# Kernel tuning notes

Hardware: AMD Instinct MI355X
Metric: run time of the kernel (lower is better)

## Reference

```python
import jax, jax.numpy as jnp
import numpy as np

LOG2PI = 1.8378770664093453
KL_WEIGHT = 1.0
N_OBS = 2_000_000
N_REFL = 250_000
N_IMG = 2000
MC = 32
N_OPS = 2
D_META = 6
D_EMB = 32
D_IN = 2 + 2 + D_META + 2 + D_EMB  # Imodel(2) + Iscale(2) + metadata(6) + wavelength + 1/d^2 + image embed
HIDDEN = 64


def weighted_pearson(x, y, w):
    z = 1.0 / w.sum(-1)
    mx = z * (w * x).sum(-1)
    my = z * (w * y).sum(-1)
    dx = x - mx
    dy = y - my
    cxy = z * (w * dx * dy).sum(-1)
    cx = z * (w * dx * dx).sum(-1)
    cy = z * (w * dy * dy).sum(-1)
    return cxy / jnp.sqrt(cx * cy)


def setup_inputs() -> dict:
    key = jax.random.key(0)
    ks = jax.random.split(key, 16)
    I = jax.random.normal(ks[0], (N_OBS, 1), jnp.float32)
    SigI = jax.random.uniform(ks[1], (N_OBS, 1), jnp.float32, 0.5, 1.5)
    image_id = jnp.sort(jax.random.randint(ks[2], (N_OBS,), 0, N_IMG, jnp.int32))
    metadata = jax.random.normal(ks[3], (N_OBS, D_META), jnp.float32)
    wavelength = 1.0 + 0.1 * jax.random.uniform(ks[4], (N_OBS, 1), jnp.float32)
    dHKL = jax.random.uniform(ks[5], (N_OBS, 1), jnp.float32, 1.0, 4.0)
    refl_ids = jax.random.randint(ks[6], (N_OPS, N_OBS), 0, N_REFL, jnp.int32)
    q_loc = jax.random.normal(ks[7], (N_REFL,), jnp.float32)
    q_scale_raw = 0.1 * jax.random.normal(ks[8], (N_REFL,), jnp.float32)
    img_emb = 0.1 * jax.random.normal(ks[9], (N_IMG, D_EMB), jnp.float32)
    W1 = jax.random.normal(ks[10], (D_IN, HIDDEN), jnp.float32) / np.sqrt(D_IN)
    b1 = jnp.zeros((HIDDEN,), jnp.float32)
    W2 = jax.random.normal(ks[11], (HIDDEN, 2), jnp.float32) / np.sqrt(HIDDEN)
    b2 = jnp.zeros((2,), jnp.float32)
    zeps = jax.random.normal(ks[12], (MC, N_REFL), jnp.float32)
    seps = jax.random.normal(ks[13], (N_OBS, MC), jnp.float32)
    return dict(I=I, SigI=SigI, image_id=image_id, metadata=metadata,
                wavelength=wavelength, dHKL=dHKL, refl_ids=refl_ids,
                q_loc=q_loc, q_scale_raw=q_scale_raw, img_emb=img_emb,
                W1=W1, b1=b1, W2=W2, b2=b2, zeps=zeps, seps=seps)


def reference(I, SigI, image_id, metadata, wavelength, dHKL, refl_ids,
              q_loc, q_scale_raw, img_emb, W1, b1, W2, b2, zeps, seps):
    n_images = img_emb.shape[0]
    sq = jax.nn.softplus(q_scale_raw)                         # q.stddev  [n_refl]
    # KL(N(q_loc, sq) || N(0, 1)), analytic, averaged over reflections
    kl_div = (-jnp.log(sq) + 0.5 * (sq * sq + q_loc * q_loc) - 0.5).mean()
    meta = jnp.concatenate([metadata, wavelength, 1.0 / jnp.square(dHKL)], -1)  # [N, 8]
    Iscale = jnp.concatenate([I, SigI], -1)                   # [N, 2]
    Imodel = jnp.stack([q_loc, sq], -1)                       # [n_refl, 2]
    zT = (q_loc[None, :] + sq[None, :] * zeps).T              # rsample, [n_refl, mc]
    emb = img_emb[image_id]                                   # [N, d_emb]
    ll_list, Ipred_list = [], []
    for op in range(refl_ids.shape[0]):                       # small fixed op count
        rid = refl_ids[op]                                    # [N]
        _Imodel = Imodel[rid]                                 # gather  [N, 2]
        feats = jnp.concatenate([_Imodel, Iscale, meta, emb], -1)
        h = jax.nn.relu(feats @ W1 + b1)
        loc_ls = h @ W2 + b2                                  # [N, 2]
        scale = loc_ls[:, :1] + jax.nn.softplus(loc_ls[:, 1:]) * seps  # [N, mc]
        _Ipred = zT[rid] * scale                              # gather * scale [N, mc]
        _ll = -0.5 * jnp.square((_Ipred - I) / SigI) - jnp.log(SigI) - 0.5 * LOG2PI
        _ll = jax.ops.segment_sum(_ll, image_id, num_segments=n_images)  # [n_img, mc]
        ll_list.append(_ll.mean(-1))                          # [n_img]
        Ipred_list.append(_Ipred.mean(-1))                    # [N]
    ll = jnp.stack(ll_list, -1)                               # [n_img, n_ops]
    ll_max = ll.max(-1)
    op_idx = ll.argmax(-1)                                    # [n_img]
    elbo = -ll_max.mean() + KL_WEIGHT * kl_div
    Ipred = jnp.stack(Ipred_list, -1)                         # [N, n_ops]
    sel = jnp.take_along_axis(Ipred, op_idx[image_id][:, None], -1)[:, 0]
    w = 1.0 / jnp.square(SigI)
    cc = weighted_pearson(I[:, 0], sel, w[:, 0])
    return jnp.stack([elbo, cc])
```

## Files before the change

kernel.cpp:

```cpp
#include <hip/hip_runtime.h>
#include <math.h>

#define N_OBS_C 2000000
#define N_REFL_C 250000
#define N_IMG_C 2000
#define MC_C 32
#define HID 64
#define NSLOT 16
#define LOG2PI_F 1.8378770664093453f


typedef float f2 __attribute__((ext_vector_type(2)));

__device__ __forceinline__ void pkfma(f2& d, f2 a, f2 b) {
    asm("v_pk_fma_f32 %0, %1, %2, %0" : "+v"(d) : "v"(a), "v"(b));
}
__device__ __forceinline__ f2 pkfma3(f2 a, f2 b, f2 c) {
    f2 d;
    asm("v_pk_fma_f32 %0, %1, %2, %3" : "=v"(d) : "v"(a), "v"(b), "v"(c));
    return d;
}

__device__ __forceinline__ float softplusf(float x) {
    return (x > 20.f) ? x : log1pf(expf(x));
}

#define ZERO_F4 96004
__global__ __launch_bounds__(256) void k_zero(float4* __restrict__ p) {
    int i = blockIdx.x * 256 + threadIdx.x;
    if (i < ZERO_F4) p[i] = make_float4(0.f, 0.f, 0.f, 0.f);
}

__global__ __launch_bounds__(256) void k_refl(const float* __restrict__ q_loc,
                                              const float* __restrict__ q_scale_raw,
                                              const float* __restrict__ zeps,
                                              float* __restrict__ sq,
                                              float* __restrict__ zT,
                                              double* __restrict__ kl_sum) {
    int r = blockIdx.x * 256 + threadIdx.x;
    double kl = 0.0;
    if (r < N_REFL_C) {
        float ql = q_loc[r];
        float sp = softplusf(q_scale_raw[r]);
        sq[r] = sp;
        kl = (double)(-logf(sp) + 0.5f * (sp * sp + ql * ql) - 0.5f);
        float z[MC_C];
#pragma unroll
        for (int m = 0; m < MC_C; ++m)
            z[m] = fmaf(sp, zeps[(size_t)m * N_REFL_C + r], ql);
        float4* outp = (float4*)(zT + (size_t)r * MC_C);
#pragma unroll
        for (int q = 0; q < MC_C / 4; ++q)
            outp[q] = make_float4(z[4 * q], z[4 * q + 1], z[4 * q + 2], z[4 * q + 3]);
    }
    for (int o = 32; o > 0; o >>= 1) kl += __shfl_xor(kl, o);
    __shared__ double skl[4];
    int lane = threadIdx.x & 63, w = threadIdx.x >> 6;
    if (lane == 0) skl[w] = kl;
    __syncthreads();
    if (threadIdx.x == 0) atomicAdd(kl_sum, skl[0] + skl[1] + skl[2] + skl[3]);
}

__global__ __launch_bounds__(64) void k_imgpre(const float* __restrict__ img_emb,
                                               const float* __restrict__ W1,
                                               const float* __restrict__ b1,
                                               float* __restrict__ img_pre) {
    int g = blockIdx.x;
    int j = threadIdx.x;
    float acc = b1[j];
#pragma unroll
    for (int e = 0; e < 32; ++e)
        acc = fmaf(img_emb[g * 32 + e], W1[(12 + e) * HID + j], acc);
    img_pre[g * HID + j] = acc;
}

__global__ __launch_bounds__(256) void k_mlp(const float* __restrict__ I,
                                             const float* __restrict__ SigI,
                                             const int* __restrict__ image_id,
                                             const float* __restrict__ metadata,
                                             const float* __restrict__ wavelength,
                                             const float* __restrict__ dHKL,
                                             const int* __restrict__ refl_ids,
                                             const float* __restrict__ q_loc,
                                             const float* __restrict__ W1,
                                             const float* __restrict__ W2,
                                             const float* __restrict__ b2,
                                             const float* __restrict__ sq,
                                             const float* __restrict__ img_pre,
                                             float4* __restrict__ params) {
    __shared__ float sW1[12 * HID];
    __shared__ float sW2a[HID], sW2b[HID];
    for (int t = threadIdx.x; t < 12 * HID; t += 256) sW1[t] = W1[t];
    if (threadIdx.x < HID) {
        sW2a[threadIdx.x] = W2[threadIdx.x * 2 + 0];
        sW2b[threadIdx.x] = W2[threadIdx.x * 2 + 1];
    }
    __syncthreads();

    int n0 = blockIdx.x * 512 + threadIdx.x;
    int n1 = n0 + 256;
    bool a0 = (n0 < N_OBS_C), a1 = (n1 < N_OBS_C);
    int m0 = a0 ? n0 : (N_OBS_C - 1);
    int m1 = a1 ? n1 : (N_OBS_C - 1);

    f2 f0p[10], f1p[10];
    {
        float v;
        v = I[m0];            f0p[0].x = v; f0p[0].y = v;
        v = SigI[m0];         f0p[1].x = v; f0p[1].y = v;
#pragma unroll
        for (int i = 0; i < 6; ++i) {
            v = metadata[(size_t)m0 * 6 + i];
            f0p[2 + i].x = v; f0p[2 + i].y = v;
        }
        v = wavelength[m0];   f0p[8].x = v; f0p[8].y = v;
        float dh = dHKL[m0];
        v = 1.0f / (dh * dh); f0p[9].x = v; f0p[9].y = v;

        v = I[m1];            f1p[0].x = v; f1p[0].y = v;
        v = SigI[m1];         f1p[1].x = v; f1p[1].y = v;
#pragma unroll
        for (int i = 0; i < 6; ++i) {
            v = metadata[(size_t)m1 * 6 + i];
            f1p[2 + i].x = v; f1p[2 + i].y = v;
        }
        v = wavelength[m1];   f1p[8].x = v; f1p[8].y = v;
        dh = dHKL[m1];
        v = 1.0f / (dh * dh); f1p[9].x = v; f1p[9].y = v;
    }

    int g0 = image_id[m0], g1 = image_id[m1];
    int r00 = refl_ids[m0], r01 = refl_ids[N_OBS_C + m0];
    int r10 = refl_ids[m1], r11 = refl_ids[N_OBS_C + m1];
    f2 qa0p, sa0p, qb0p, sb0p, qa1p, sa1p, qb1p, sb1p;
    { float v;
      v = q_loc[r00]; qa0p.x = v; qa0p.y = v;
      v = sq[r00];    sa0p.x = v; sa0p.y = v;
      v = q_loc[r01]; qb0p.x = v; qb0p.y = v;
      v = sq[r01];    sb0p.x = v; sb0p.y = v;
      v = q_loc[r10]; qa1p.x = v; qa1p.y = v;
      v = sq[r10];    sa1p.x = v; sa1p.y = v;
      v = q_loc[r11]; qb1p.x = v; qb1p.y = v;
      v = sq[r11];    sb1p.x = v; sb1p.y = v;
    }
    const float* ip0 = img_pre + (size_t)g0 * HID;
    const float* ip1 = img_pre + (size_t)g1 * HID;

    f2 lA00 = {0.f, 0.f}, lA01 = {0.f, 0.f}, lB00 = {0.f, 0.f}, lB01 = {0.f, 0.f};
    f2 lA10 = {0.f, 0.f}, lA11 = {0.f, 0.f}, lB10 = {0.f, 0.f}, lB11 = {0.f, 0.f};

#pragma unroll 1
    for (int jt = 0; jt < HID; jt += 8) {
        f2 ac0[4], ac1[4];
        {
            float4 pa = *(const float4*)&ip0[jt];
            float4 pb = *(const float4*)&ip0[jt + 4];
            ac0[0].x = pa.x; ac0[0].y = pa.y;
            ac0[1].x = pa.z; ac0[1].y = pa.w;
            ac0[2].x = pb.x; ac0[2].y = pb.y;
            ac0[3].x = pb.z; ac0[3].y = pb.w;
            pa = *(const float4*)&ip1[jt];
            pb = *(const float4*)&ip1[jt + 4];
            ac1[0].x = pa.x; ac1[0].y = pa.y;
            ac1[1].x = pa.z; ac1[1].y = pa.w;
            ac1[2].x = pb.x; ac1[2].y = pb.y;
            ac1[3].x = pb.z; ac1[3].y = pb.w;
        }
#pragma unroll
        for (int i = 0; i < 10; ++i) {
            float4 wa = *(const float4*)&sW1[(i + 2) * HID + jt];
            float4 wb = *(const float4*)&sW1[(i + 2) * HID + jt + 4];
            f2 w0; w0.x = wa.x; w0.y = wa.y;
            f2 w1; w1.x = wa.z; w1.y = wa.w;
            f2 w2; w2.x = wb.x; w2.y = wb.y;
            f2 w3; w3.x = wb.z; w3.y = wb.w;
            pkfma(ac0[0], f0p[i], w0); pkfma(ac1[0], f1p[i], w0);
            pkfma(ac0[1], f0p[i], w1); pkfma(ac1[1], f1p[i], w1);
            pkfma(ac0[2], f0p[i], w2); pkfma(ac1[2], f1p[i], w2);
            pkfma(ac0[3], f0p[i], w3); pkfma(ac1[3], f1p[i], w3);
        }
        f2 w0p[4], w1p[4], vap[4], vbp[4];
        {
            float4 wa = *(const float4*)&sW1[jt];
            float4 wb = *(const float4*)&sW1[jt + 4];
            w0p[0].x = wa.x; w0p[0].y = wa.y;
            w0p[1].x = wa.z; w0p[1].y = wa.w;
            w0p[2].x = wb.x; w0p[2].y = wb.y;
            w0p[3].x = wb.z; w0p[3].y = wb.w;
            wa = *(const float4*)&sW1[HID + jt];
            wb = *(const float4*)&sW1[HID + jt + 4];
            w1p[0].x = wa.x; w1p[0].y = wa.y;
            w1p[1].x = wa.z; w1p[1].y = wa.w;
            w1p[2].x = wb.x; w1p[2].y = wb.y;
            w1p[3].x = wb.z; w1p[3].y = wb.w;
            wa = *(const float4*)&sW2a[jt];
            wb = *(const float4*)&sW2a[jt + 4];
            vap[0].x = wa.x; vap[0].y = wa.y;
            vap[1].x = wa.z; vap[1].y = wa.w;
            vap[2].x = wb.x; vap[2].y = wb.y;
            vap[3].x = wb.z; vap[3].y = wb.w;
            wa = *(const float4*)&sW2b[jt];
            wb = *(const float4*)&sW2b[jt + 4];
            vbp[0].x = wa.x; vbp[0].y = wa.y;
            vbp[1].x = wa.z; vbp[1].y = wa.w;
            vbp[2].x = wb.x; vbp[2].y = wb.y;
            vbp[3].x = wb.z; vbp[3].y = wb.w;
        }
#pragma unroll
        for (int k = 0; k < 4; ++k) {
            f2 h;
            h = pkfma3(sa0p, w1p[k], ac0[k]);
            pkfma(h, qa0p, w0p[k]);
            h.x = fmaxf(h.x, 0.f); h.y = fmaxf(h.y, 0.f);
            pkfma(lA00, h, vap[k]);
            pkfma(lA01, h, vbp[k]);
            h = pkfma3(sb0p, w1p[k], ac0[k]);
            pkfma(h, qb0p, w0p[k]);
            h.x = fmaxf(h.x, 0.f); h.y = fmaxf(h.y, 0.f);
            pkfma(lB00, h, vap[k]);
            pkfma(lB01, h, vbp[k]);
            h = pkfma3(sa1p, w1p[k], ac1[k]);
            pkfma(h, qa1p, w0p[k]);
            h.x = fmaxf(h.x, 0.f); h.y = fmaxf(h.y, 0.f);
            pkfma(lA10, h, vap[k]);
            pkfma(lA11, h, vbp[k]);
            h = pkfma3(sb1p, w1p[k], ac1[k]);
            pkfma(h, qb1p, w0p[k]);
            h.x = fmaxf(h.x, 0.f); h.y = fmaxf(h.y, 0.f);
            pkfma(lB10, h, vap[k]);
            pkfma(lB11, h, vbp[k]);
        }
    }

    float bb0 = b2[0], bb1 = b2[1];
    if (a0) {
        float la0 = bb0 + lA00.x + lA00.y;
        float la1 = bb1 + lA01.x + lA01.y;
        float lb0 = bb0 + lB00.x + lB00.y;
        float lb1 = bb1 + lB01.x + lB01.y;
        params[n0] = make_float4(la0, softplusf(la1), lb0, softplusf(lb1));
    }
    if (a1) {
        float la0 = bb0 + lA10.x + lA10.y;
        float la1 = bb1 + lA11.x + lA11.y;
        float lb0 = bb0 + lB10.x + lB10.y;
        float lb1 = bb1 + lB11.x + lB11.y;
        params[n1] = make_float4(la0, softplusf(la1), lb0, softplusf(lb1));
    }
}

__global__ __launch_bounds__(256) void k_mc(const float* __restrict__ I,
                                            const float* __restrict__ SigI,
                                            const int* __restrict__ image_id,
                                            const int* __restrict__ refl_ids,
                                            const float4* __restrict__ params,
                                            const float* __restrict__ seps,
                                            const float* __restrict__ zT,
                                            float* __restrict__ img_mom) {
    int t = threadIdx.x;
    int grp = t >> 3;
    int m4 = t & 7;
    int n = blockIdx.x * 32 + grp;

    float In = I[n];
    float Sn = SigI[n];
    int g = image_id[n];
    int rid0 = refl_ids[n];
    int rid1 = refl_ids[N_OBS_C + n];
    float4 pp = params[n];

    float4 ss = *(const float4*)&seps[(size_t)n * MC_C + m4 * 4];
    float4 z0 = *(const float4*)&zT[(size_t)rid0 * MC_C + m4 * 4];
    float4 z1 = *(const float4*)&zT[(size_t)rid1 * MC_C + m4 * 4];

    float rsig = 1.0f / Sn;
    float mnIr = -In * rsig;

    float sd20 = 0.f, sip0 = 0.f, sd21 = 0.f, sip1 = 0.f;
#define MCSTEP(zc0, zc1, sc_)                              \
    {                                                      \
        float sc0 = fmaf(pp.y, sc_, pp.x);                 \
        float ip0 = zc0 * sc0;                             \
        float d0 = fmaf(ip0, rsig, mnIr);                  \
        sd20 = fmaf(d0, d0, sd20);                         \
        sip0 += ip0;                                       \
        float sc1 = fmaf(pp.w, sc_, pp.z);                 \
        float ip1 = zc1 * sc1;                             \
        float d1 = fmaf(ip1, rsig, mnIr);                  \
        sd21 = fmaf(d1, d1, sd21);                         \
        sip1 += ip1;                                       \
    }
    MCSTEP(z0.x, z1.x, ss.x)
    MCSTEP(z0.y, z1.y, ss.y)
    MCSTEP(z0.z, z1.z, ss.z)
    MCSTEP(z0.w, z1.w, ss.w)
#undef MCSTEP

#pragma unroll
    for (int o = 4; o > 0; o >>= 1) {
        sd20 += __shfl_xor(sd20, o);
        sd21 += __shfl_xor(sd21, o);
        sip0 += __shfl_xor(sip0, o);
        sip1 += __shfl_xor(sip1, o);
    }

    __shared__ float mom[12][33];
    __shared__ int sg[32];
    if (m4 == 0) {
        float logS32 = 32.f * logf(Sn) + 16.f * LOG2PI_F;
        float y0 = sip0 * (1.0f / 32.0f);
        float y1 = sip1 * (1.0f / 32.0f);
        float w = rsig * rsig;
        mom[0][grp] = -0.5f * sd20 - logS32;
        mom[1][grp] = -0.5f * sd21 - logS32;
        mom[2][grp] = w;
        mom[3][grp] = w * In;
        mom[4][grp] = w * In * In;
        mom[5][grp] = w * y0;
        mom[6][grp] = w * y0 * y0;
        mom[7][grp] = w * In * y0;
        mom[8][grp] = w * y1;
        mom[9][grp] = w * y1 * y1;
        mom[10][grp] = w * In * y1;
        mom[11][grp] = 0.f;
        sg[grp] = g;
    }
    __syncthreads();
    if (t < 64) {
        int s = t & 31;
        int half = t >> 5;
        int gs = sg[s];
        int gfirst = sg[0];
        unsigned long long bal = __ballot(gs == gfirst);
        bool allsame = (bal == 0xFFFFFFFFFFFFFFFFull);
        int slot = blockIdx.x & (NSLOT - 1);
#pragma unroll
        for (int jj = 0; jj < 6; ++jj) {
            int j = jj * 2 + half;
            float v = mom[j][s];
            if (allsame) {
#pragma unroll
                for (int o = 16; o > 0; o >>= 1) v += __shfl_xor(v, o);
                if (s == 0) atomicAdd(&img_mom[(gfirst * 12 + j) * NSLOT + slot], v);
            } else {
                atomicAdd(&img_mom[(gs * 12 + j) * NSLOT + slot], v);
            }
        }
    }
}

__global__ __launch_bounds__(256) void k_img(const float* __restrict__ img_mom,
                                             double* __restrict__ accs) {
    int g = blockIdx.x * 256 + threadIdx.x;
    double red7[7] = {0, 0, 0, 0, 0, 0, 0};
    if (g < N_IMG_C) {
        float M[12];
#pragma unroll
        for (int j = 0; j < 12; ++j) {
            const float4* p = (const float4*)&img_mom[(g * 12 + j) * NSLOT];
            float4 q0 = p[0], q1 = p[1], q2 = p[2], q3 = p[3];
            M[j] = (q0.x + q0.y + q0.z + q0.w) + (q1.x + q1.y + q1.z + q1.w) +
                   (q2.x + q2.y + q2.z + q2.w) + (q3.x + q3.y + q3.z + q3.w);
        }
        float ll0 = M[0] * (1.0f / 32.0f);
        float ll1 = M[1] * (1.0f / 32.0f);
        bool op1 = (ll1 > ll0);
        red7[0] = (double)fmaxf(ll0, ll1);
        red7[1] = (double)M[2];
        red7[2] = (double)M[3];
        red7[3] = (double)(op1 ? M[8] : M[5]);
        red7[4] = (double)M[4];
        red7[5] = (double)(op1 ? M[9] : M[6]);
        red7[6] = (double)(op1 ? M[10] : M[7]);
    }
#pragma unroll
    for (int k = 0; k < 7; ++k)
        for (int o = 32; o > 0; o >>= 1) red7[k] += __shfl_xor(red7[k], o);
    __shared__ double sred[4][7];
    int lane = threadIdx.x & 63, w = threadIdx.x >> 6;
    if (lane == 0) {
#pragma unroll
        for (int k = 0; k < 7; ++k) sred[w][k] = red7[k];
    }
    __syncthreads();
    if (threadIdx.x < 7) {
        double v = sred[0][threadIdx.x] + sred[1][threadIdx.x] +
                   sred[2][threadIdx.x] + sred[3][threadIdx.x];
        atomicAdd(&accs[1 + threadIdx.x], v);
    }
}

__global__ void k_final(const double* __restrict__ accs, float* __restrict__ out) {
    double kl = accs[0] / (double)N_REFL_C;
    double elbo = -(accs[1] / (double)N_IMG_C) + 1.0 * kl;
    double W = accs[2], Sx = accs[3], Sy = accs[4];
    double Sxx = accs[5], Syy = accs[6], Sxy = accs[7];
    double z = 1.0 / W;
    double mx = z * Sx, my = z * Sy;
    double cxy = z * Sxy - mx * my;
    double cx = z * Sxx - mx * mx;
    double cy = z * Syy - my * my;
    double cc = cxy / sqrt(cx * cy);
    out[0] = (float)elbo;
    out[1] = (float)cc;
}

extern "C" void kernel_launch(void* const* d_in, const int* in_sizes, int n_in,
                              void* d_out, int out_size, void* d_ws, size_t ws_size,
                              hipStream_t stream) {
    const float* I = (const float*)d_in[0];
    const float* SigI = (const float*)d_in[1];
    const int* image_id = (const int*)d_in[2];
    const float* metadata = (const float*)d_in[3];
    const float* wavelength = (const float*)d_in[4];
    const float* dHKL = (const float*)d_in[5];
    const int* refl_ids = (const int*)d_in[6];
    const float* q_loc = (const float*)d_in[7];
    const float* q_scale_raw = (const float*)d_in[8];
    const float* img_emb = (const float*)d_in[9];
    const float* W1 = (const float*)d_in[10];
    const float* b1 = (const float*)d_in[11];
    const float* W2 = (const float*)d_in[12];
    const float* b2 = (const float*)d_in[13];
    const float* zeps = (const float*)d_in[14];
    const float* seps = (const float*)d_in[15];
    float* out = (float*)d_out;

    char* ws = (char*)d_ws;
    double* accs = (double*)ws;
    float* img_mom = (float*)(ws + 64);
    float* sqv = (float*)(ws + 2097152);
    float* img_pre = (float*)(ws + 4194304);
    float* zT = (float*)(ws + 8388608);
    float4* params = (float4*)(ws + 50331648);

    k_zero<<<(ZERO_F4 + 255) / 256, 256, 0, stream>>>((float4*)ws);
    k_refl<<<(N_REFL_C + 255) / 256, 256, 0, stream>>>(q_loc, q_scale_raw, zeps,
                                                       sqv, zT, &accs[0]);
    k_imgpre<<<N_IMG_C, 64, 0, stream>>>(img_emb, W1, b1, img_pre);
    k_mlp<<<(N_OBS_C + 511) / 512, 256, 0, stream>>>(I, SigI, image_id, metadata,
                                                     wavelength, dHKL, refl_ids,
                                                     q_loc, W1, W2, b2, sqv,
                                                     img_pre, params);
    k_mc<<<N_OBS_C / 32, 256, 0, stream>>>(I, SigI, image_id, refl_ids,
                                           params, seps, zT, img_mom);
    k_img<<<(N_IMG_C + 255) / 256, 256, 0, stream>>>(img_mom, accs);
    k_final<<<1, 1, 0, stream>>>(accs, out);
}
```

Baseline: 287.8 us.

## Fuse MLP and Monte Carlo kernels via shared-memory params and block-local image reduction

Merges the per-observation MLP kernel and the Monte Carlo likelihood kernel into one kernel. The per-observation params now stay in shared memory, so the params array is no longer written to and re-read from global memory. Each thread now handles one observation instead of two. Image moment partial sums are accumulated with shared-memory atomics, indexed relative to the block's first image, and flushed once per block; images at offset 32 or more fall back to global atomics. The costs are halved ILP in the MLP section, more shared-memory atomics, and extra sync and occupancy pressure in the fused kernel.

```diff
diff --git a/kernel.cpp b/kernel.cpp
--- a/kernel.cpp
+++ b/kernel.cpp
@@ -74,97 +74,82 @@
     img_pre[g * HID + j] = acc;
 }
 
-__global__ __launch_bounds__(256) void k_mlp(const float* __restrict__ I,
-                                             const float* __restrict__ SigI,
-                                             const int* __restrict__ image_id,
-                                             const float* __restrict__ metadata,
-                                             const float* __restrict__ wavelength,
-                                             const float* __restrict__ dHKL,
-                                             const int* __restrict__ refl_ids,
-                                             const float* __restrict__ q_loc,
-                                             const float* __restrict__ W1,
-                                             const float* __restrict__ W2,
-                                             const float* __restrict__ b2,
-                                             const float* __restrict__ sq,
-                                             const float* __restrict__ img_pre,
-                                             float4* __restrict__ params) {
+__global__ __launch_bounds__(256) void k_main(const float* __restrict__ I,
+                                              const float* __restrict__ SigI,
+                                              const int* __restrict__ image_id,
+                                              const float* __restrict__ metadata,
+                                              const float* __restrict__ wavelength,
+                                              const float* __restrict__ dHKL,
+                                              const int* __restrict__ refl_ids,
+                                              const float* __restrict__ q_loc,
+                                              const float* __restrict__ W1,
+                                              const float* __restrict__ W2,
+                                              const float* __restrict__ b2,
+                                              const float* __restrict__ sq,
+                                              const float* __restrict__ img_pre,
+                                              const float* __restrict__ seps,
+                                              const float* __restrict__ zT,
+                                              float* __restrict__ img_mom) {
     __shared__ float sW1[12 * HID];
     __shared__ float sW2a[HID], sW2b[HID];
-    for (int t = threadIdx.x; t < 12 * HID; t += 256) sW1[t] = W1[t];
-    if (threadIdx.x < HID) {
-        sW2a[threadIdx.x] = W2[threadIdx.x * 2 + 0];
-        sW2b[threadIdx.x] = W2[threadIdx.x * 2 + 1];
-    }
-    __syncthreads();
-
-    int n0 = blockIdx.x * 512 + threadIdx.x;
-    int n1 = n0 + 256;
-    bool a0 = (n0 < N_OBS_C), a1 = (n1 < N_OBS_C);
-    int m0 = a0 ? n0 : (N_OBS_C - 1);
-    int m1 = a1 ? n1 : (N_OBS_C - 1);
-
-    f2 f0p[10], f1p[10];
+    __shared__ float4 pms[256];
+    __shared__ float2 sIS[256];
+    __shared__ int2 srid[256];
+    __shared__ int sgid[256];
+    __shared__ float lmom[32][12];
+
+    int tid = threadIdx.x;
+    for (int t = tid; t < 12 * HID; t += 256) sW1[t] = W1[t];
+    if (tid < HID) {
+        sW2a[tid] = W2[tid * 2 + 0];
+        sW2b[tid] = W2[tid * 2 + 1];
+    }
+    for (int t = tid; t < 32 * 12; t += 256) ((float*)lmom)[t] = 0.f;
+
+    int n = blockIdx.x * 256 + tid;
+    bool act = (n < N_OBS_C);
+    int m = act ? n : (N_OBS_C - 1);
+
+    float Inv = I[m];
+    float Snv = SigI[m];
+    f2 fp[10];
     {
         float v;
-        v = I[m0];            f0p[0].x = v; f0p[0].y = v;
-        v = SigI[m0];         f0p[1].x = v; f0p[1].y = v;
+        fp[0].x = Inv; fp[0].y = Inv;
+        fp[1].x = Snv; fp[1].y = Snv;
 #pragma unroll
         for (int i = 0; i < 6; ++i) {
-            v = metadata[(size_t)m0 * 6 + i];
-            f0p[2 + i].x = v; f0p[2 + i].y = v;
-        }
-        v = wavelength[m0];   f0p[8].x = v; f0p[8].y = v;
-        float dh = dHKL[m0];
-        v = 1.0f / (dh * dh); f0p[9].x = v; f0p[9].y = v;
-
-        v = I[m1];            f1p[0].x = v; f1p[0].y = v;
-        v = SigI[m1];         f1p[1].x = v; f1p[1].y = v;
-#pragma unroll
-        for (int i = 0; i < 6; ++i) {
-            v = metadata[(size_t)m1 * 6 + i];
-            f1p[2 + i].x = v; f1p[2 + i].y = v;
-        }
-        v = wavelength[m1];   f1p[8].x = v; f1p[8].y = v;
-        dh = dHKL[m1];
-        v = 1.0f / (dh * dh); f1p[9].x = v; f1p[9].y = v;
-    }
-
-    int g0 = image_id[m0], g1 = image_id[m1];
-    int r00 = refl_ids[m0], r01 = refl_ids[N_OBS_C + m0];
-    int r10 = refl_ids[m1], r11 = refl_ids[N_OBS_C + m1];
-    f2 qa0p, sa0p, qb0p, sb0p, qa1p, sa1p, qb1p, sb1p;
+            v = metadata[(size_t)m * 6 + i];
+            fp[2 + i].x = v; fp[2 + i].y = v;
+        }
+        v = wavelength[m]; fp[8].x = v; fp[8].y = v;
+        float dh = dHKL[m];
+        v = 1.0f / (dh * dh); fp[9].x = v; fp[9].y = v;
+    }
+    int g = image_id[m];
+    int r0 = refl_ids[m];
+    int r1 = refl_ids[N_OBS_C + m];
+    f2 qa, sa, qb, sb;
     { float v;
-      v = q_loc[r00]; qa0p.x = v; qa0p.y = v;
-      v = sq[r00];    sa0p.x = v; sa0p.y = v;
-      v = q_loc[r01]; qb0p.x = v; qb0p.y = v;
-      v = sq[r01];    sb0p.x = v; sb0p.y = v;
-      v = q_loc[r10]; qa1p.x = v; qa1p.y = v;
-      v = sq[r10];    sa1p.x = v; sa1p.y = v;
-      v = q_loc[r11]; qb1p.x = v; qb1p.y = v;
-      v = sq[r11];    sb1p.x = v; sb1p.y = v;
-    }
-    const float* ip0 = img_pre + (size_t)g0 * HID;
-    const float* ip1 = img_pre + (size_t)g1 * HID;
-
-    f2 lA00 = {0.f, 0.f}, lA01 = {0.f, 0.f}, lB00 = {0.f, 0.f}, lB01 = {0.f, 0.f};
-    f2 lA10 = {0.f, 0.f}, lA11 = {0.f, 0.f}, lB10 = {0.f, 0.f}, lB11 = {0.f, 0.f};
+      v = q_loc[r0]; qa.x = v; qa.y = v;
+      v = sq[r0];    sa.x = v; sa.y = v;
+      v = q_loc[r1]; qb.x = v; qb.y = v;
+      v = sq[r1];    sb.x = v; sb.y = v;
+    }
+    const float* ipg = img_pre + (size_t)g * HID;
+
+    f2 lA0 = {0.f, 0.f}, lA1 = {0.f, 0.f}, lB0 = {0.f, 0.f}, lB1 = {0.f, 0.f};
 
 #pragma unroll 1
     for (int jt = 0; jt < HID; jt += 8) {
-        f2 ac0[4], ac1[4];
+        f2 ac[4];
         {
-            float4 pa = *(const float4*)&ip0[jt];
-            float4 pb = *(const float4*)&ip0[jt + 4];
-            ac0[0].x = pa.x; ac0[0].y = pa.y;
-            ac0[1].x = pa.z; ac0[1].y = pa.w;
-            ac0[2].x = pb.x; ac0[2].y = pb.y;
-            ac0[3].x = pb.z; ac0[3].y = pb.w;
-            pa = *(const float4*)&ip1[jt];
-            pb = *(const float4*)&ip1[jt + 4];
-            ac1[0].x = pa.x; ac1[0].y = pa.y;
-            ac1[1].x = pa.z; ac1[1].y = pa.w;
-            ac1[2].x = pb.x; ac1[2].y = pb.y;
-            ac1[3].x = pb.z; ac1[3].y = pb.w;
+            float4 pa = *(const float4*)&ipg[jt];
+            float4 pb = *(const float4*)&ipg[jt + 4];
+            ac[0].x = pa.x; ac[0].y = pa.y;
+            ac[1].x = pa.z; ac[1].y = pa.w;
+            ac[2].x = pb.x; ac[2].y = pb.y;
+            ac[3].x = pb.z; ac[3].y = pb.w;
         }
 #pragma unroll
         for (int i = 0; i < 10; ++i) {
@@ -174,10 +159,10 @@
             f2 w1; w1.x = wa.z; w1.y = wa.w;
             f2 w2; w2.x = wb.x; w2.y = wb.y;
             f2 w3; w3.x = wb.z; w3.y = wb.w;
-            pkfma(ac0[0], f0p[i], w0); pkfma(ac1[0], f1p[i], w0);
-            pkfma(ac0[1], f0p[i], w1); pkfma(ac1[1], f1p[i], w1);
-            pkfma(ac0[2], f0p[i], w2); pkfma(ac1[2], f1p[i], w2);
-            pkfma(ac0[3], f0p[i], w3); pkfma(ac1[3], f1p[i], w3);
+            pkfma(ac[0], fp[i], w0);
+            pkfma(ac[1], fp[i], w1);
+            pkfma(ac[2], fp[i], w2);
+            pkfma(ac[3], fp[i], w3);
         }
         f2 w0p[4], w1p[4], vap[4], vbp[4];
         {
@@ -209,142 +194,114 @@
 #pragma unroll
         for (int k = 0; k < 4; ++k) {
             f2 h;
-            h = pkfma3(sa0p, w1p[k], ac0[k]);
-            pkfma(h, qa0p, w0p[k]);
+            h = pkfma3(sa, w1p[k], ac[k]);
+            pkfma(h, qa, w0p[k]);
             h.x = fmaxf(h.x, 0.f); h.y = fmaxf(h.y, 0.f);
-            pkfma(lA00, h, vap[k]);
-            pkfma(lA01, h, vbp[k]);
-            h = pkfma3(sb0p, w1p[k], ac0[k]);
-            pkfma(h, qb0p, w0p[k]);
+            pkfma(lA0, h, vap[k]);
+            pkfma(lA1, h, vbp[k]);
+            h = pkfma3(sb, w1p[k], ac[k]);
+            pkfma(h, qb, w0p[k]);
             h.x = fmaxf(h.x, 0.f); h.y = fmaxf(h.y, 0.f);
-            pkfma(lB00, h, vap[k]);
-            pkfma(lB01, h, vbp[k]);
-            h = pkfma3(sa1p, w1p[k], ac1[k]);
-            pkfma(h, qa1p, w0p[k]);
-            h.x = fmaxf(h.x, 0.f); h.y = fmaxf(h.y, 0.f);
-            pkfma(lA10, h, vap[k]);
-            pkfma(lA11, h, vbp[k]);
-            h = pkfma3(sb1p, w1p[k], ac1[k]);
-            pkfma(h, qb1p, w0p[k]);
-            h.x = fmaxf(h.x, 0.f); h.y = fmaxf(h.y, 0.f);
-            pkfma(lB10, h, vap[k]);
-            pkfma(lB11, h, vbp[k]);
-        }
-    }
-
-    float bb0 = b2[0], bb1 = b2[1];
-    if (a0) {
-        float la0 = bb0 + lA00.x + lA00.y;
-        float la1 = bb1 + lA01.x + lA01.y;
-        float lb0 = bb0 + lB00.x + lB00.y;
-        float lb1 = bb1 + lB01.x + lB01.y;
-        params[n0] = make_float4(la0, softplusf(la1), lb0, softplusf(lb1));
-    }
-    if (a1) {
-        float la0 = bb0 + lA10.x + lA10.y;
-        float la1 = bb1 + lA11.x + lA11.y;
-        float lb0 = bb0 + lB10.x + lB10.y;
-        float lb1 = bb1 + lB11.x + lB11.y;
-        params[n1] = make_float4(la0, softplusf(la1), lb0, softplusf(lb1));
-    }
-}
-
-__global__ __launch_bounds__(256) void k_mc(const float* __restrict__ I,
-                                            const float* __restrict__ SigI,
-                                            const int* __restrict__ image_id,
-                                            const int* __restrict__ refl_ids,
-                                            const float4* __restrict__ params,
-                                            const float* __restrict__ seps,
-                                            const float* __restrict__ zT,
-                                            float* __restrict__ img_mom) {
-    int t = threadIdx.x;
-    int grp = t >> 3;
-    int m4 = t & 7;
-    int n = blockIdx.x * 32 + grp;
-
-    float In = I[n];
-    float Sn = SigI[n];
-    int g = image_id[n];
-    int rid0 = refl_ids[n];
-    int rid1 = refl_ids[N_OBS_C + n];
-    float4 pp = params[n];
-
-    float4 ss = *(const float4*)&seps[(size_t)n * MC_C + m4 * 4];
-    float4 z0 = *(const float4*)&zT[(size_t)rid0 * MC_C + m4 * 4];
-    float4 z1 = *(const float4*)&zT[(size_t)rid1 * MC_C + m4 * 4];
-
-    float rsig = 1.0f / Sn;
-    float mnIr = -In * rsig;
-
-    float sd20 = 0.f, sip0 = 0.f, sd21 = 0.f, sip1 = 0.f;
+            pkfma(lB0, h, vap[k]);
+            pkfma(lB1, h, vbp[k]);
+        }
+    }
+
+    {
+        float bb0 = b2[0], bb1 = b2[1];
+        float la0 = bb0 + lA0.x + lA0.y;
+        float la1 = bb1 + lA1.x + lA1.y;
+        float lb0 = bb0 + lB0.x + lB0.y;
+        float lb1 = bb1 + lB1.x + lB1.y;
+        pms[tid] = make_float4(la0, softplusf(la1), lb0, softplusf(lb1));
+        sIS[tid] = make_float2(Inv, Snv);
+        srid[tid] = make_int2(r0, r1);
+        sgid[tid] = act ? g : -1;
+    }
+    __syncthreads();
+
+    int grp = tid >> 3;
+    int m4 = tid & 7;
+    int gmin = sgid[0];
+    int slot = blockIdx.x & (NSLOT - 1);
+
+#pragma unroll 2
+    for (int c = 0; c < 8; ++c) {
+        int o = c * 32 + grp;
+        int gb = sgid[o];
+        int2 rr = srid[o];
+        float4 pp = pms[o];
+        float2 IS = sIS[o];
+        int nb = (gb >= 0) ? (blockIdx.x * 256 + o) : 0;
+
+        float4 ss = *(const float4*)&seps[(size_t)nb * MC_C + m4 * 4];
+        float4 z0 = *(const float4*)&zT[(size_t)rr.x * MC_C + m4 * 4];
+        float4 z1 = *(const float4*)&zT[(size_t)rr.y * MC_C + m4 * 4];
+
+        float rsig = 1.0f / IS.y;
+        float mnIr = -IS.x * rsig;
+
+        float sd20 = 0.f, sip0 = 0.f, sd21 = 0.f, sip1 = 0.f;
 #define MCSTEP(zc0, zc1, sc_)                              \
-    {                                                      \
-        float sc0 = fmaf(pp.y, sc_, pp.x);                 \
-        float ip0 = zc0 * sc0;                             \
-        float d0 = fmaf(ip0, rsig, mnIr);                  \
-        sd20 = fmaf(d0, d0, sd20);                         \
-        sip0 += ip0;                                       \
-        float sc1 = fmaf(pp.w, sc_, pp.z);                 \
-        float ip1 = zc1 * sc1;                             \
-        float d1 = fmaf(ip1, rsig, mnIr);                  \
-        sd21 = fmaf(d1, d1, sd21);                         \
-        sip1 += ip1;                                       \
-    }
-    MCSTEP(z0.x, z1.x, ss.x)
-    MCSTEP(z0.y, z1.y, ss.y)
-    MCSTEP(z0.z, z1.z, ss.z)
-    MCSTEP(z0.w, z1.w, ss.w)
+        {                                                  \
+            float sc0 = fmaf(pp.y, sc_, pp.x);             \
+            float ip0 = zc0 * sc0;                         \
+            float d0 = fmaf(ip0, rsig, mnIr);              \
+            sd20 = fmaf(d0, d0, sd20);                     \
+            sip0 += ip0;                                   \
+            float sc1 = fmaf(pp.w, sc_, pp.z);             \
+            float ip1 = zc1 * sc1;                         \
+            float d1 = fmaf(ip1, rsig, mnIr);              \
+            sd21 = fmaf(d1, d1, sd21);                     \
+            sip1 += ip1;                                   \
+        }
+        MCSTEP(z0.x, z1.x, ss.x)
+        MCSTEP(z0.y, z1.y, ss.y)
+        MCSTEP(z0.z, z1.z, ss.z)
+        MCSTEP(z0.w, z1.w, ss.w)
 #undef MCSTEP
 
 #pragma unroll
-    for (int o = 4; o > 0; o >>= 1) {
-        sd20 += __shfl_xor(sd20, o);
-        sd21 += __shfl_xor(sd21, o);
-        sip0 += __shfl_xor(sip0, o);
-        sip1 += __shfl_xor(sip1, o);
-    }
-
-    __shared__ float mom[12][33];
-    __shared__ int sg[32];
-    if (m4 == 0) {
-        float logS32 = 32.f * logf(Sn) + 16.f * LOG2PI_F;
-        float y0 = sip0 * (1.0f / 32.0f);
-        float y1 = sip1 * (1.0f / 32.0f);
-        float w = rsig * rsig;
-        mom[0][grp] = -0.5f * sd20 - logS32;
-        mom[1][grp] = -0.5f * sd21 - logS32;
-        mom[2][grp] = w;
-        mom[3][grp] = w * In;
-        mom[4][grp] = w * In * In;
-        mom[5][grp] = w * y0;
-        mom[6][grp] = w * y0 * y0;
-        mom[7][grp] = w * In * y0;
-        mom[8][grp] = w * y1;
-        mom[9][grp] = w * y1 * y1;
-        mom[10][grp] = w * In * y1;
-        mom[11][grp] = 0.f;
-        sg[grp] = g;
+        for (int o2 = 4; o2 > 0; o2 >>= 1) {
+            sd20 += __shfl_xor(sd20, o2);
+            sd21 += __shfl_xor(sd21, o2);
+            sip0 += __shfl_xor(sip0, o2);
+            sip1 += __shfl_xor(sip1, o2);
+        }
+
+        if (gb >= 0) {
+            float logS32 = 32.f * logf(IS.y) + 16.f * LOG2PI_F;
+            float y0 = sip0 * (1.0f / 32.0f);
+            float y1 = sip1 * (1.0f / 32.0f);
+            float w = rsig * rsig;
+            float mv0, mv1 = 0.f;
+            switch (m4) {
+                case 0: mv0 = -0.5f * sd20 - logS32; mv1 = w * y1;        break;
+                case 1: mv0 = -0.5f * sd21 - logS32; mv1 = w * y1 * y1;   break;
+                case 2: mv0 = w;                     mv1 = w * IS.x * y1; break;
+                case 3: mv0 = w * IS.x;                                   break;
+                case 4: mv0 = w * IS.x * IS.x;                            break;
+                case 5: mv0 = w * y0;                                     break;
+                case 6: mv0 = w * y0 * y0;                                break;
+                default: mv0 = w * IS.x * y0;                             break;
+            }
+            int loc = gb - gmin;
+            if (loc < 32) {
+                atomicAdd(&lmom[loc][m4], mv0);
+                if (m4 < 3) atomicAdd(&lmom[loc][m4 + 8], mv1);
+            } else {
+                atomicAdd(&img_mom[(gb * 12 + m4) * NSLOT + slot], mv0);
+                if (m4 < 3) atomicAdd(&img_mom[(gb * 12 + m4 + 8) * NSLOT + slot], mv1);
+            }
+        }
     }
     __syncthreads();
-    if (t < 64) {
-        int s = t & 31;
-        int half = t >> 5;
-        int gs = sg[s];
-        int gfirst = sg[0];
-        unsigned long long bal = __ballot(gs == gfirst);
-        bool allsame = (bal == 0xFFFFFFFFFFFFFFFFull);
-        int slot = blockIdx.x & (NSLOT - 1);
-#pragma unroll
-        for (int jj = 0; jj < 6; ++jj) {
-            int j = jj * 2 + half;
-            float v = mom[j][s];
-            if (allsame) {
-#pragma unroll
-                for (int o = 16; o > 0; o >>= 1) v += __shfl_xor(v, o);
-                if (s == 0) atomicAdd(&img_mom[(gfirst * 12 + j) * NSLOT + slot], v);
-            } else {
-                atomicAdd(&img_mom[(gs * 12 + j) * NSLOT + slot], v);
-            }
+
+    for (int t = tid; t < 32 * 12; t += 256) {
+        float v = ((float*)lmom)[t];
+        if (v != 0.f) {
+            int loc = t / 12, j = t - loc * 12;
+            atomicAdd(&img_mom[((gmin + loc) * 12 + j) * NSLOT + slot], v);
         }
     }
 }
@@ -432,18 +389,15 @@
     float* sqv = (float*)(ws + 2097152);
     float* img_pre = (float*)(ws + 4194304);
     float* zT = (float*)(ws + 8388608);
-    float4* params = (float4*)(ws + 50331648);
 
     k_zero<<<(ZERO_F4 + 255) / 256, 256, 0, stream>>>((float4*)ws);
     k_refl<<<(N_REFL_C + 255) / 256, 256, 0, stream>>>(q_loc, q_scale_raw, zeps,
                                                        sqv, zT, &accs[0]);
     k_imgpre<<<N_IMG_C, 64, 0, stream>>>(img_emb, W1, b1, img_pre);
-    k_mlp<<<(N_OBS_C + 511) / 512, 256, 0, stream>>>(I, SigI, image_id, metadata,
-                                                     wavelength, dHKL, refl_ids,
-                                                     q_loc, W1, W2, b2, sqv,
-                                                     img_pre, params);
-    k_mc<<<N_OBS_C / 32, 256, 0, stream>>>(I, SigI, image_id, refl_ids,
-                                           params, seps, zT, img_mom);
+    k_main<<<(N_OBS_C + 255) / 256, 256, 0, stream>>>(I, SigI, image_id, metadata,
+                                                      wavelength, dHKL, refl_ids,
+                                                      q_loc, W1, W2, b2, sqv,
+                                                      img_pre, seps, zT, img_mom);
     k_img<<<(N_IMG_C + 255) / 256, 256, 0, stream>>>(img_mom, accs);
     k_final<<<1, 1, 0, stream>>>(accs, out);
 }
```

After: 295.4 us. 2.6% more time.
